# Kernel optimization log

Measured on AMD Instinct MI355X. Metric: run time of the kernel, lower is better.

The kernel has to match this reference:

```python
import jax, jax.numpy as jnp
from jax import lax
import numpy as np

R, C = 1536, 1536


def setup_inputs() -> dict:
    key = jax.random.key(0)
    # binary mask: nonzero = foreground (gets a distance), zero = background
    mask = jax.random.randint(key, (R, C), 0, 2).astype(jnp.float32)
    return {"mask": mask}


def reference(mask):
    """Exact Euclidean distance transform, matching scipy.ndimage.distance_transform_edt.

    Two-phase separable (Meijster) algorithm:
      phase 1: per-column 1D distance (in rows) to nearest background pixel
      phase 2: per-row min-plus combine: D2[i,j] = min_k (g[i,k]^2 + (j-k)^2)
    Phase 2 is done as an exact vectorized min-plus against a [C,C] offset
    matrix, scanned over rows to bound memory.
    """
    n_rows, n_cols = mask.shape
    BIG = jnp.float32(n_rows + n_cols)  # > any achievable grid distance
    bg = (mask == 0)  # background => distance 0

    # ---- phase 1: vertical 1D distance per column ----
    def col_step(carry, row_bg):
        d = jnp.where(row_bg, jnp.float32(0.0), jnp.minimum(carry + 1.0, BIG))
        return d, d

    init = jnp.full((n_cols,), BIG, dtype=jnp.float32)
    _, down = lax.scan(col_step, init, bg)                 # top -> bottom
    _, up = lax.scan(col_step, init, bg, reverse=True)     # bottom -> top
    g = jnp.minimum(down, up)                              # [R, C]
    g2 = g * g

    # ---- phase 2: horizontal min-plus per row ----
    idx = jnp.arange(n_cols, dtype=jnp.float32)
    jk2 = (idx[:, None] - idx[None, :]) ** 2               # [C(j), C(k)]

    def row_step(_, g2_row):
        d2 = jnp.min(g2_row[None, :] + jk2, axis=1)        # [C]
        return None, d2

    _, d2 = lax.scan(row_step, None, g2)                   # [R, C]
    return jnp.sqrt(d2)
```

## Files before the change

kernel.cpp:

```cpp
#include <hip/hip_runtime.h>
#include <math.h>


#define RR   1536
#define CC   1536
#define BIGF 3072.0f
#define BIG2 9437184.0f
#define H    6
#define NCH  256
#define TILE 256
#define W    128
#define NT   (CC / TILE)

__global__ __launch_bounds__(256) void edt_sum(
    const float* __restrict__ mask,
    unsigned* __restrict__ bits)
{
    const int col2 = blockIdx.x * 256 + threadIdx.x;
    const int ch   = blockIdx.y;
    const float2* __restrict__ p =
        (const float2*)(mask + (size_t)(ch * H) * CC) + col2;
    unsigned w0 = 0, w1 = 0;
    #pragma unroll
    for (int ri = 0; ri < H; ++ri) {
        float2 m = p[ri * (CC / 2)];
        if (m.x == 0.0f) w0 |= (1u << ri);
        if (m.y == 0.0f) w1 |= (1u << ri);
    }
    bits[ch * CC + 2 * col2]     = w0;
    bits[ch * CC + 2 * col2 + 1] = w1;
}

__global__ __launch_bounds__(256) void edt_carry(
    const unsigned* __restrict__ bits,
    float* __restrict__ CD,
    float* __restrict__ CU)
{
    const int col = blockIdx.x;
    const int t   = threadIdx.x;
    __shared__ float Pm[NCH], Pn[NCH];

    unsigned w = bits[t * CC + col];
    float a, b;
    if (w) {
        a = (float)__builtin_ctz(w);
        b = (float)(H - 1 - (31 - __builtin_clz(w)));
    } else {
        a = BIGF; b = BIGF;
    }
    Pm[t]           = b - (float)(t * H);
    Pn[NCH - 1 - t] = a + (float)(t * H);
    __syncthreads();

    #pragma unroll
    for (int off = 1; off < NCH; off <<= 1) {
        float vm, vn;
        if (t >= off) {
            vm = fminf(Pm[t], Pm[t - off]);
            vn = fminf(Pn[t], Pn[t - off]);
        }
        __syncthreads();
        if (t >= off) { Pm[t] = vm; Pn[t] = vn; }
        __syncthreads();
    }

    float cd = (t == 0) ? BIGF
             : fminf(Pm[t - 1] + (float)((t - 1) * H), BIGF + (float)(t * H));
    float cu = (t == NCH - 1) ? BIGF
             : fminf(Pn[NCH - 2 - t] - (float)((t + 1) * H),
                     BIGF + (float)((NCH - 1 - t) * H));
    CD[t * CC + col] = cd;
    CU[t * CC + col] = cu;
}

__global__ __launch_bounds__(256) void edt_strip(
    const unsigned* __restrict__ bits,
    const float* __restrict__ CD,
    const float* __restrict__ CU,
    float* __restrict__ out)
{
    __shared__ float g2[H][TILE + 2 * W];
    const int ch = blockIdx.y;
    const int tx = blockIdx.x;
    const int t  = threadIdx.x;
    const int c0 = tx * TILE - W;

    #pragma unroll
    for (int m = 0; m < 2; ++m) {
        const int lc = t + m * 256;
        const int c  = c0 + lc;
        if (c >= 0 && c < CC) {
            const unsigned w = bits[ch * CC + c];
            float d[H];
            float prev = CD[ch * CC + c];
            #pragma unroll
            for (int ri = 0; ri < H; ++ri) {
                bool bg = (w >> ri) & 1u;
                float dd = bg ? 0.0f : fminf(prev + 1.0f, BIGF);
                d[ri] = dd;
                prev = dd;
            }
            float up = CU[ch * CC + c];
            #pragma unroll
            for (int ri = H - 1; ri >= 0; --ri) {
                bool bg = (w >> ri) & 1u;
                float u = bg ? 0.0f : fminf(up + 1.0f, BIGF);
                up = u;
                float g = fminf(d[ri], u);
                g2[ri][lc] = g * g;
            }
        } else {
            #pragma unroll
            for (int ri = 0; ri < H; ++ri) g2[ri][lc] = BIG2;
        }
    }
    __syncthreads();

    float* __restrict__ obase = out + (size_t)(ch * H) * CC + tx * TILE;
    const int lj = t + W;
    #pragma unroll
    for (int r = 0; r < H; ++r) {
        float best = g2[r][lj];
        int dk = 1;
        while (dk <= W && (float)(dk * dk) < best) {
            float dk2 = (float)(dk * dk);
            best = fminf(best, g2[r][lj - dk] + dk2);
            best = fminf(best, g2[r][lj + dk] + dk2);
            ++dk;
        }
        obase[r * CC + t] = sqrtf(best);
    }
}

extern "C" void kernel_launch(void* const* d_in, const int* in_sizes, int n_in,
                              void* d_out, int out_size, void* d_ws, size_t ws_size,
                              hipStream_t stream) {
    const float* mask = (const float*)d_in[0];
    float* out = (float*)d_out;

    unsigned* bits = (unsigned*)d_ws;
    float* CD = (float*)(bits + NCH * CC);
    float* CU = CD + NCH * CC;

    edt_sum  <<<dim3(CC / 512, NCH), 256, 0, stream>>>(mask, bits);
    edt_carry<<<CC, NCH, 0, stream>>>(bits, CD, CU);
    edt_strip<<<dim3(NT, NCH), 256, 0, stream>>>(bits, CD, CU, out);
}
```

Before: 77.28 us.

## Fuse three EDT kernels into one persistent kernel with grid-wide atomic barrier

Merges the bit-packing, column carry scan and strip min-plus kernels into one launch of 1536 blocks. A software grid barrier (atomic counter plus spin with s_sleep) separates the carry phase from the strip phase, and a memset resets the counter on each call. The bit-packing now reads the mask with per-column scalar loads inside the carry block instead of vectorized float2 rows. This aims to remove two kernel launch gaps, but it depends on all 1536 blocks being co-resident (occupancy hint of 6 blocks per CU) to avoid deadlock, and it adds the cost of the barrier and the memset.

```diff
diff --git a/kernel.cpp b/kernel.cpp
--- a/kernel.cpp
+++ b/kernel.cpp
@@ -11,124 +11,129 @@
 #define TILE 256
 #define W    128
 #define NT   (CC / TILE)
+#define NBLK 1536
 
-__global__ __launch_bounds__(256) void edt_sum(
+struct __align__(16) Smem {
+    union {
+        struct { float Pm[NCH]; float Pn[NCH]; } scan;
+        float g2[H][TILE + 2 * W];
+    };
+};
+
+__global__ __launch_bounds__(256, 6) void edt_fused(
     const float* __restrict__ mask,
-    unsigned* __restrict__ bits)
+    unsigned* __restrict__ bits,
+    float* __restrict__ CD,
+    float* __restrict__ CU,
+    unsigned* __restrict__ bar,
+    float* __restrict__ out)
 {
-    const int col2 = blockIdx.x * 256 + threadIdx.x;
-    const int ch   = blockIdx.y;
-    const float2* __restrict__ p =
-        (const float2*)(mask + (size_t)(ch * H) * CC) + col2;
-    unsigned w0 = 0, w1 = 0;
-    #pragma unroll
-    for (int ri = 0; ri < H; ++ri) {
-        float2 m = p[ri * (CC / 2)];
-        if (m.x == 0.0f) w0 |= (1u << ri);
-        if (m.y == 0.0f) w1 |= (1u << ri);
-    }
-    bits[ch * CC + 2 * col2]     = w0;
-    bits[ch * CC + 2 * col2 + 1] = w1;
-}
+    __shared__ Smem sm;
+    const int b = blockIdx.x;
+    const int t = threadIdx.x;
 
-__global__ __launch_bounds__(256) void edt_carry(
-    const unsigned* __restrict__ bits,
-    float* __restrict__ CD,
-    float* __restrict__ CU)
-{
-    const int col = blockIdx.x;
-    const int t   = threadIdx.x;
-    __shared__ float Pm[NCH], Pn[NCH];
+    {
+        const int col = b;
+        const float* __restrict__ p = mask + (size_t)(t * H) * CC + col;
+        unsigned w = 0;
+        #pragma unroll
+        for (int ri = 0; ri < H; ++ri)
+            if (p[ri * CC] == 0.0f) w |= (1u << ri);
+        bits[t * CC + col] = w;
 
-    unsigned w = bits[t * CC + col];
-    float a, b;
-    if (w) {
-        a = (float)__builtin_ctz(w);
-        b = (float)(H - 1 - (31 - __builtin_clz(w)));
-    } else {
-        a = BIGF; b = BIGF;
-    }
-    Pm[t]           = b - (float)(t * H);
-    Pn[NCH - 1 - t] = a + (float)(t * H);
-    __syncthreads();
+        float a, bb;
+        if (w) {
+            a  = (float)__builtin_ctz(w);
+            bb = (float)(H - 1 - (31 - __builtin_clz(w)));
+        } else {
+            a = BIGF; bb = BIGF;
+        }
+        sm.scan.Pm[t]           = bb - (float)(t * H);
+        sm.scan.Pn[NCH - 1 - t] = a  + (float)(t * H);
+        __syncthreads();
 
-    #pragma unroll
-    for (int off = 1; off < NCH; off <<= 1) {
-        float vm, vn;
-        if (t >= off) {
-            vm = fminf(Pm[t], Pm[t - off]);
-            vn = fminf(Pn[t], Pn[t - off]);
+        #pragma unroll
+        for (int off = 1; off < NCH; off <<= 1) {
+            float vm, vn;
+            if (t >= off) {
+                vm = fminf(sm.scan.Pm[t], sm.scan.Pm[t - off]);
+                vn = fminf(sm.scan.Pn[t], sm.scan.Pn[t - off]);
+            }
+            __syncthreads();
+            if (t >= off) { sm.scan.Pm[t] = vm; sm.scan.Pn[t] = vn; }
+            __syncthreads();
         }
-        __syncthreads();
-        if (t >= off) { Pm[t] = vm; Pn[t] = vn; }
-        __syncthreads();
+
+        float cd = (t == 0) ? BIGF
+                 : fminf(sm.scan.Pm[t - 1] + (float)((t - 1) * H),
+                         BIGF + (float)(t * H));
+        float cu = (t == NCH - 1) ? BIGF
+                 : fminf(sm.scan.Pn[NCH - 2 - t] - (float)((t + 1) * H),
+                         BIGF + (float)((NCH - 1 - t) * H));
+        CD[t * CC + col] = cd;
+        CU[t * CC + col] = cu;
     }
 
-    float cd = (t == 0) ? BIGF
-             : fminf(Pm[t - 1] + (float)((t - 1) * H), BIGF + (float)(t * H));
-    float cu = (t == NCH - 1) ? BIGF
-             : fminf(Pn[NCH - 2 - t] - (float)((t + 1) * H),
-                     BIGF + (float)((NCH - 1 - t) * H));
-    CD[t * CC + col] = cd;
-    CU[t * CC + col] = cu;
-}
-
-__global__ __launch_bounds__(256) void edt_strip(
-    const unsigned* __restrict__ bits,
-    const float* __restrict__ CD,
-    const float* __restrict__ CU,
-    float* __restrict__ out)
-{
-    __shared__ float g2[H][TILE + 2 * W];
-    const int ch = blockIdx.y;
-    const int tx = blockIdx.x;
-    const int t  = threadIdx.x;
-    const int c0 = tx * TILE - W;
-
-    #pragma unroll
-    for (int m = 0; m < 2; ++m) {
-        const int lc = t + m * 256;
-        const int c  = c0 + lc;
-        if (c >= 0 && c < CC) {
-            const unsigned w = bits[ch * CC + c];
-            float d[H];
-            float prev = CD[ch * CC + c];
-            #pragma unroll
-            for (int ri = 0; ri < H; ++ri) {
-                bool bg = (w >> ri) & 1u;
-                float dd = bg ? 0.0f : fminf(prev + 1.0f, BIGF);
-                d[ri] = dd;
-                prev = dd;
-            }
-            float up = CU[ch * CC + c];
-            #pragma unroll
-            for (int ri = H - 1; ri >= 0; --ri) {
-                bool bg = (w >> ri) & 1u;
-                float u = bg ? 0.0f : fminf(up + 1.0f, BIGF);
-                up = u;
-                float g = fminf(d[ri], u);
-                g2[ri][lc] = g * g;
-            }
-        } else {
-            #pragma unroll
-            for (int ri = 0; ri < H; ++ri) g2[ri][lc] = BIG2;
-        }
+    __syncthreads();
+    if (t == 0) {
+        __threadfence();
+        atomicAdd(bar, 1u);
+        while (atomicAdd(bar, 0u) < NBLK)
+            __builtin_amdgcn_s_sleep(16);
+        __threadfence();
     }
     __syncthreads();
 
-    float* __restrict__ obase = out + (size_t)(ch * H) * CC + tx * TILE;
-    const int lj = t + W;
-    #pragma unroll
-    for (int r = 0; r < H; ++r) {
-        float best = g2[r][lj];
-        int dk = 1;
-        while (dk <= W && (float)(dk * dk) < best) {
-            float dk2 = (float)(dk * dk);
-            best = fminf(best, g2[r][lj - dk] + dk2);
-            best = fminf(best, g2[r][lj + dk] + dk2);
-            ++dk;
+    {
+        const int ch = b & (NCH - 1);
+        const int tx = b >> 8;
+        const int c0 = tx * TILE - W;
+
+        #pragma unroll
+        for (int m = 0; m < 2; ++m) {
+            const int lc = t + m * 256;
+            const int c  = c0 + lc;
+            if (c >= 0 && c < CC) {
+                const unsigned w = bits[ch * CC + c];
+                float d[H];
+                float prev = CD[ch * CC + c];
+                #pragma unroll
+                for (int ri = 0; ri < H; ++ri) {
+                    bool bg = (w >> ri) & 1u;
+                    float dd = bg ? 0.0f : fminf(prev + 1.0f, BIGF);
+                    d[ri] = dd;
+                    prev = dd;
+                }
+                float up = CU[ch * CC + c];
+                #pragma unroll
+                for (int ri = H - 1; ri >= 0; --ri) {
+                    bool bg = (w >> ri) & 1u;
+                    float u = bg ? 0.0f : fminf(up + 1.0f, BIGF);
+                    up = u;
+                    float g = fminf(d[ri], u);
+                    sm.g2[ri][lc] = g * g;
+                }
+            } else {
+                #pragma unroll
+                for (int ri = 0; ri < H; ++ri) sm.g2[ri][lc] = BIG2;
+            }
         }
-        obase[r * CC + t] = sqrtf(best);
+        __syncthreads();
+
+        float* __restrict__ obase = out + (size_t)(ch * H) * CC + tx * TILE;
+        const int lj = t + W;
+        #pragma unroll
+        for (int r = 0; r < H; ++r) {
+            float best = sm.g2[r][lj];
+            int dk = 1;
+            while (dk <= W && (float)(dk * dk) < best) {
+                float dk2 = (float)(dk * dk);
+                best = fminf(best, sm.g2[r][lj - dk] + dk2);
+                best = fminf(best, sm.g2[r][lj + dk] + dk2);
+                ++dk;
+            }
+            obase[r * CC + t] = sqrtf(best);
+        }
     }
 }
 
@@ -141,8 +146,8 @@
     unsigned* bits = (unsigned*)d_ws;
     float* CD = (float*)(bits + NCH * CC);
     float* CU = CD + NCH * CC;
+    unsigned* bar = (unsigned*)((char*)d_ws + (32u << 20));
 
-    edt_sum  <<<dim3(CC / 512, NCH), 256, 0, stream>>>(mask, bits);
-    edt_carry<<<CC, NCH, 0, stream>>>(bits, CD, CU);
-    edt_strip<<<dim3(NT, NCH), 256, 0, stream>>>(bits, CD, CU, out);
+    hipMemsetAsync(bar, 0, 256, stream);
+    edt_fused<<<NBLK, 256, 0, stream>>>(mask, bits, CD, CU, bar, out);
 }
```

Measured after the change: 302.8 us. +291.8%, slower.
